# Kernel optimization log

Hardware: AMD Instinct MI355X
Metric: run time of the kernel (lower is better)

The kernel has to match this reference:

```python
import jax, jax.numpy as jnp
import numpy as np

N = 65536      # total nodes (512 graphs x 128 agents)
E = 524288     # total edges (avg degree 8)
NPG = 128      # nodes per graph
OBS = 256      # dim_in_node + dim_in_u
HID = 512      # hidden_dim
MID = 256      # dim_mid
LSTM = 256     # dim_lstm_out
DOUT = 128     # dim_out
DLAST = 128    # dim_last
RFM = 256      # rfm_hidden_dim
LH = 256       # last_hidden
ACT = 8        # act_dims


def setup_inputs() -> dict:
    key = jax.random.key(0)
    ks = jax.random.split(key, 30)

    def rn(k, shape, fan_in):
        return jax.random.normal(k, shape, jnp.float32) * (1.0 / np.sqrt(fan_in))

    src = jax.random.randint(ks[3], (E,), 0, N, jnp.int32)
    # keep edges inside each 128-node graph (batched-graph semantics)
    dst = (src // NPG) * NPG + jax.random.randint(ks[4], (E,), 0, NPG, jnp.int32)

    inp = {
        "obs": jax.random.normal(ks[0], (N, OBS), jnp.float32),
        "h0": jax.random.normal(ks[1], (N, LSTM), jnp.float32) * 0.1,
        "c0": jax.random.normal(ks[2], (N, LSTM), jnp.float32) * 0.1,
        "src": src,
        "dst": dst,
        # mlp1a / mlp1b
        "w1a": rn(ks[5], (HID, OBS), OBS), "b1a": jnp.zeros((HID,), jnp.float32),
        "w1b": rn(ks[6], (MID, HID), HID), "b1b": jnp.zeros((MID,), jnp.float32),
        # lstm1 (gate order i,f,g,o as in torch)
        "w_ih": rn(ks[7], (4 * LSTM, MID), MID), "b_ih": jnp.zeros((4 * LSTM,), jnp.float32),
        "w_hh": rn(ks[8], (4 * LSTM, LSTM), LSTM), "b_hh": jnp.zeros((4 * LSTM,), jnp.float32),
        # mlp1
        "w1": rn(ks[9], (DOUT, LSTM), LSTM), "b1": jnp.zeros((DOUT,), jnp.float32),
        # RFMBlock edge MLP (input = src_nf ++ dst_nf = 2*DOUT; edge_feat/u are 0-dim)
        "we": rn(ks[10], (RFM, 2 * DOUT), 2 * DOUT), "be": jnp.zeros((RFM,), jnp.float32),
        "we2": rn(ks[11], (DLAST, RFM), RFM), "be2": jnp.zeros((DLAST,), jnp.float32),
        # RFMBlock node MLP (input = node_feat ++ h = DOUT + DLAST)
        "wn": rn(ks[12], (RFM, DOUT + DLAST), DOUT + DLAST), "bn": jnp.zeros((RFM,), jnp.float32),
        "wn2": rn(ks[13], (DLAST, RFM), RFM), "bn2": jnp.zeros((DLAST,), jnp.float32),
        # readout
        "wr": rn(ks[14], (LH, DLAST), DLAST), "br": jnp.zeros((LH,), jnp.float32),
        "wr2": rn(ks[15], (ACT, LH), LH), "br2": jnp.zeros((ACT,), jnp.float32),
    }
    return inp


def reference(obs, h0, c0, src, dst,
              w1a, b1a, w1b, b1b, w_ih, b_ih, w_hh, b_hh, w1, b1,
              we, be, we2, be2, wn, bn, wn2, bn2, wr, br, wr2, br2):
    # node encoder: mlp1b(relu(mlp1a(obs)))
    x = jnp.maximum(obs @ w1a.T + b1a, 0.0) @ w1b.T + b1b            # [N, MID]
    # single-step LSTM (batch = N nodes, seq_len = 1)
    gates = x @ w_ih.T + h0 @ w_hh.T + (b_ih + b_hh)                 # [N, 4*LSTM]
    i, f, g, o = jnp.split(gates, 4, axis=-1)
    c1 = jax.nn.sigmoid(f) * c0 + jax.nn.sigmoid(i) * jnp.tanh(g)
    h1 = jax.nn.sigmoid(o) * jnp.tanh(c1)
    nf = jnp.maximum(h1, 0.0) @ w1.T + b1                            # [N, DOUT]

    # RFMBlock edge update: fc_edge2(relu(fc_edge([src_nf, dst_nf])))
    einp = jnp.concatenate([nf[src], nf[dst]], axis=-1)              # [E, 2*DOUT]
    ef = jnp.maximum(einp @ we.T + be, 0.0) @ we2.T + be2            # [E, DLAST]

    # message = edge_feat, reduce = sum over incoming edges (by dst)
    agg = jax.ops.segment_sum(ef, dst, num_segments=N)               # [N, DLAST]

    # RFMBlock node update: fc_node2(relu(fc_node([node_feat, h])))
    ninp = jnp.concatenate([nf, agg], axis=-1)                       # [N, DOUT+DLAST]
    nf2 = jnp.maximum(ninp @ wn.T + bn, 0.0) @ wn2.T + bn2           # [N, DLAST]

    # readout: mlp1_readout2(relu(mlp1_readout(n_out)))
    logits = jnp.maximum(nf2 @ wr.T + br, 0.0) @ wr2.T + br2         # [N, ACT]
    return logits, h1, c1
```

## Files before the change

kernel.cpp:

```cpp
#include <hip/hip_runtime.h>
#include <cstdint>
#include <cstddef>


#define NN 65536
#define NE 524288

typedef __bf16 bf16x8 __attribute__((ext_vector_type(8)));
typedef float  f32x4  __attribute__((ext_vector_type(4)));

typedef __attribute__((address_space(1))) unsigned int glb_uint;
typedef __attribute__((address_space(3))) unsigned int lds_uint;

__device__ __forceinline__ void async16(const void* g, void* l){
  __builtin_amdgcn_global_load_lds((glb_uint*)g, (lds_uint*)l, 16, 0, 0);
}

__device__ __forceinline__ float bf2f(unsigned short u){
  union { unsigned int i; float f; } v; v.i = ((unsigned int)u) << 16; return v.f;
}
__device__ __forceinline__ unsigned short f2b(float f){
  union { float f; unsigned int i; } v; v.f = f;
  unsigned int r = v.i + 0x7FFFu + ((v.i >> 16) & 1u);
  return (unsigned short)(r >> 16);
}
__device__ __forceinline__ float sigm(float x){ return 1.f/(1.f+__expf(-x)); }

struct ConvArgs {
  const float* s[14];
  unsigned short* d[14];
  int n4[14];
  int cnt;
};

__global__ __launch_bounds__(256) void convert_kernel(ConvArgs a){
  int stride = gridDim.x * blockDim.x;
  int gid = blockIdx.x * blockDim.x + threadIdx.x;
  for (int seg = 0; seg < a.cnt; ++seg){
    const float4* s = (const float4*)a.s[seg];
    ushort4* d = (ushort4*)a.d[seg];
    int n4 = a.n4[seg];
    for (int i = gid; i < n4; i += stride){
      float4 v = s[i];
      ushort4 o; o.x=f2b(v.x); o.y=f2b(v.y); o.z=f2b(v.z); o.w=f2b(v.w);
      d[i] = o;
    }
  }
}

template<int ACT, int RSCALE>
__global__ __launch_bounds__(256) void gemm_kernel(
    const unsigned short* __restrict__ A, int lda,
    const unsigned short* __restrict__ B, int ldb, int K,
    const float* __restrict__ bias,
    const int* __restrict__ rs,
    unsigned short* __restrict__ C, int ldc)
{
  __shared__ alignas(16) unsigned short As[2][4096];
  __shared__ alignas(16) unsigned short Bs[2][4096];
  int t = threadIdx.x, wave = t >> 6, lane = t & 63;
  int m0 = blockIdx.x * 128, n0 = blockIdx.y * 128;
  int wr = wave >> 1, wc = wave & 1;

  f32x4 acc[4][4] = {};

  int srow = lane & 15, schunk = lane >> 4;
  const unsigned short* Ap0 = A + (size_t)(m0 + wave * 16 + srow) * lda + schunk * 8;
  const unsigned short* Ap1 = Ap0 + (size_t)64 * lda;
  const unsigned short* Bp0 = B + (size_t)(n0 + wave * 16 + srow) * ldb + schunk * 8;
  const unsigned short* Bp1 = Bp0 + (size_t)64 * ldb;

  auto stage = [&](int b, int kt){
    async16(Ap0 + kt, &As[b][(wave)     << 9]);
    async16(Ap1 + kt, &As[b][(wave + 4) << 9]);
    async16(Bp0 + kt, &Bs[b][(wave)     << 9]);
    async16(Bp1 + kt, &Bs[b][(wave + 4) << 9]);
  };
  int fo = (schunk << 7) + (srow << 3);
  auto compute = [&](int b){
    bf16x8 av[4], bv[4];
#pragma unroll
    for (int m = 0; m < 4; ++m) av[m] = *(const bf16x8*)&As[b][((wr * 4 + m) << 9) + fo];
#pragma unroll
    for (int n = 0; n < 4; ++n) bv[n] = *(const bf16x8*)&Bs[b][((wc * 4 + n) << 9) + fo];
#pragma unroll
    for (int m = 0; m < 4; ++m)
#pragma unroll
      for (int n = 0; n < 4; ++n)
        acc[m][n] = __builtin_amdgcn_mfma_f32_16x16x32_bf16(av[m], bv[n], acc[m][n], 0, 0, 0);
  };

  stage(0, 0);
  asm volatile("s_waitcnt vmcnt(0)" ::: "memory");
  __builtin_amdgcn_s_barrier();
  int cur = 0;
  for (int kt = 32; kt < K; kt += 32){
    stage(cur ^ 1, kt);
    asm volatile("s_waitcnt vmcnt(4)" ::: "memory");
    __builtin_amdgcn_sched_barrier(0);
    __builtin_amdgcn_s_barrier();
    compute(cur);
    asm volatile("s_waitcnt lgkmcnt(0)" ::: "memory");
    __builtin_amdgcn_s_barrier();
    cur ^= 1;
  }
  asm volatile("s_waitcnt vmcnt(0)" ::: "memory");
  __builtin_amdgcn_sched_barrier(0);
  __builtin_amdgcn_s_barrier();
  compute(cur);

  int coll = lane & 15, rq = lane >> 4;
#pragma unroll
  for (int n = 0; n < 4; ++n){
    int col = n0 + wc * 64 + n * 16 + coll;
    float bv = bias[col];
#pragma unroll
    for (int m = 0; m < 4; ++m){
#pragma unroll
      for (int r = 0; r < 4; ++r){
        int rrow = m0 + wr * 64 + m * 16 + rq * 4 + r;
        float scale = RSCALE ? (float)rs[rrow] : 1.0f;
        float v = acc[m][n][r] + bv * scale;
        if (ACT) v = fmaxf(v, 0.f);
        C[(size_t)rrow * ldc + col] = f2b(v);
      }
    }
  }
}

__global__ __launch_bounds__(256) void gates_lstm_kernel(
    const unsigned short* __restrict__ Xb,
    const unsigned short* __restrict__ H0b,
    const unsigned short* __restrict__ Wih,
    const unsigned short* __restrict__ Whh,
    const float* __restrict__ b_ih, const float* __restrict__ b_hh,
    const float* __restrict__ c0,
    float* __restrict__ h1o, float* __restrict__ c1o,
    unsigned short* __restrict__ rb)
{
  __shared__ alignas(16) unsigned short As[2][2048];
  __shared__ alignas(16) unsigned short Bs[2][4][2048];
  int t = threadIdx.x, wave = t >> 6, lane = t & 63;
  int m0 = blockIdx.x * 64, cb = blockIdx.y * 64;
  int srow = lane & 15, schunk = lane >> 4;

  f32x4 acc[4][4] = {};

  auto stage = [&](int b, int kt){
    const unsigned short* Abase = (kt < 256) ? (Xb + kt) : (H0b + (kt - 256));
    const unsigned short* Wbase = (kt < 256) ? (Wih + kt) : (Whh + (kt - 256));
    async16(Abase + (size_t)(m0 + wave * 16 + srow) * 256 + schunk * 8, &As[b][wave << 9]);
#pragma unroll
    for (int g = 0; g < 4; ++g)
      async16(Wbase + (size_t)(g * 256 + cb + wave * 16 + srow) * 256 + schunk * 8,
              &Bs[b][g][wave << 9]);
  };
  int fo = (schunk << 7) + (srow << 3);
  auto compute = [&](int b){
    bf16x8 a = *(const bf16x8*)&As[b][(wave << 9) + fo];
#pragma unroll
    for (int g = 0; g < 4; ++g){
#pragma unroll
      for (int j = 0; j < 4; ++j){
        bf16x8 bb = *(const bf16x8*)&Bs[b][g][(j << 9) + fo];
        acc[g][j] = __builtin_amdgcn_mfma_f32_16x16x32_bf16(a, bb, acc[g][j], 0, 0, 0);
      }
    }
  };

  stage(0, 0);
  asm volatile("s_waitcnt vmcnt(0)" ::: "memory");
  __builtin_amdgcn_s_barrier();
  int cur = 0;
  for (int kt = 32; kt < 512; kt += 32){
    stage(cur ^ 1, kt);
    asm volatile("s_waitcnt vmcnt(5)" ::: "memory");
    __builtin_amdgcn_sched_barrier(0);
    __builtin_amdgcn_s_barrier();
    compute(cur);
    asm volatile("s_waitcnt lgkmcnt(0)" ::: "memory");
    __builtin_amdgcn_s_barrier();
    cur ^= 1;
  }
  asm volatile("s_waitcnt vmcnt(0)" ::: "memory");
  __builtin_amdgcn_sched_barrier(0);
  __builtin_amdgcn_s_barrier();
  compute(cur);

  int coll = lane & 15, rq = lane >> 4;
#pragma unroll
  for (int j = 0; j < 4; ++j){
    int col = cb + j * 16 + coll;
    float bi  = b_ih[col]       + b_hh[col];
    float bff = b_ih[256 + col] + b_hh[256 + col];
    float bg  = b_ih[512 + col] + b_hh[512 + col];
    float bo  = b_ih[768 + col] + b_hh[768 + col];
#pragma unroll
    for (int r = 0; r < 4; ++r){
      int node = m0 + wave * 16 + rq * 4 + r;
      size_t off = (size_t)node * 256 + col;
      float iv = sigm(acc[0][j][r] + bi);
      float fv = sigm(acc[1][j][r] + bff);
      float gv = tanhf(acc[2][j][r] + bg);
      float ov = sigm(acc[3][j][r] + bo);
      float cv = fv * c0[off] + iv * gv;
      float hv = ov * tanhf(cv);
      h1o[off] = hv;
      c1o[off] = cv;
      rb[off] = f2b(fmaxf(hv, 0.f));
    }
  }
}

__global__ __launch_bounds__(256) void hist_kernel(
    const int* __restrict__ dst, int* __restrict__ hist)
{
  int e = blockIdx.x * 256 + threadIdx.x;
  atomicAdd(&hist[dst[e]], 1);
}

__global__ __launch_bounds__(256) void scan1_kernel(
    const int* __restrict__ hist, int* __restrict__ offs, int* __restrict__ bsum)
{
  __shared__ int s[256];
  int b = blockIdx.x, t = threadIdx.x;
  int v = hist[b * 256 + t];
  s[t] = v; __syncthreads();
  for (int d = 1; d < 256; d <<= 1){
    int x = (t >= d) ? s[t - d] : 0;
    __syncthreads();
    s[t] += x;
    __syncthreads();
  }
  offs[b * 256 + t] = s[t] - v;
  if (t == 255) bsum[b] = s[255];
}

__global__ __launch_bounds__(256) void scan2_kernel(int* __restrict__ bsum){
  __shared__ int s[256];
  int t = threadIdx.x;
  int v = bsum[t];
  s[t] = v; __syncthreads();
  for (int d = 1; d < 256; d <<= 1){
    int x = (t >= d) ? s[t - d] : 0;
    __syncthreads();
    s[t] += x;
    __syncthreads();
  }
  bsum[t] = s[t] - v;
}

__global__ __launch_bounds__(256) void scan3_kernel(
    int* __restrict__ offs, const int* __restrict__ bsum, int* __restrict__ cursor)
{
  int i = blockIdx.x * 256 + threadIdx.x;
  int v = offs[i] + bsum[blockIdx.x];
  offs[i] = v;
  cursor[i] = v;
}

__global__ __launch_bounds__(256) void scatter_kernel(
    const int* __restrict__ src, const int* __restrict__ dst,
    int* __restrict__ cursor, int* __restrict__ sorted_src)
{
  int e = blockIdx.x * 256 + threadIdx.x;
  int d = dst[e];
  int pos = atomicAdd(&cursor[d], 1);
  sorted_src[pos] = src[e];
}

__global__ __launch_bounds__(256) void edge_agg_kernel(
    const unsigned short* __restrict__ P,
    const unsigned short* __restrict__ Q,
    const int* __restrict__ sorted_src,
    const int* __restrict__ offs,
    const int* __restrict__ cnt,
    unsigned short* __restrict__ Hsum)
{
  int t = threadIdx.x;
  int n = (blockIdx.x << 2) + (t >> 6);
  int lane = t & 63;
  int d0 = lane * 4;
  int off = offs[n], c = cnt[n];
  ushort4 qv = *(const ushort4*)&Q[(size_t)n * 256 + d0];
  float q0 = bf2f(qv.x), q1 = bf2f(qv.y), q2 = bf2f(qv.z), q3 = bf2f(qv.w);
  float a0 = 0.f, a1 = 0.f, a2 = 0.f, a3 = 0.f;
  for (int i = 0; i < c; ++i){
    int s = sorted_src[off + i];
    ushort4 pv = *(const ushort4*)&P[(size_t)s * 256 + d0];
    a0 += fmaxf(bf2f(pv.x) + q0, 0.f);
    a1 += fmaxf(bf2f(pv.y) + q1, 0.f);
    a2 += fmaxf(bf2f(pv.z) + q2, 0.f);
    a3 += fmaxf(bf2f(pv.w) + q3, 0.f);
  }
  ushort4 o; o.x = f2b(a0); o.y = f2b(a1); o.z = f2b(a2); o.w = f2b(a3);
  *(ushort4*)&Hsum[(size_t)n * 256 + d0] = o;
}

__global__ __launch_bounds__(256) void logits_kernel(
    const unsigned short* __restrict__ rh,
    const unsigned short* __restrict__ wr2b,
    const float* __restrict__ br2,
    float* __restrict__ out)
{
  __shared__ alignas(16) unsigned short W[2048];
  int t = threadIdx.x;
  *(uint4*)&W[t * 8] = *(const uint4*)&wr2b[t * 8];
  __syncthreads();
  int node = blockIdx.x * 32 + (t >> 3);
  int o = t & 7;
  const unsigned short* r = rh + (size_t)node * 256;
  float s = br2[o];
#pragma unroll
  for (int k = 0; k < 256; k += 8){
    uint4 av = *(const uint4*)&r[k];
    const unsigned short* ap = (const unsigned short*)&av;
#pragma unroll
    for (int i = 0; i < 8; ++i) s += bf2f(ap[i]) * bf2f(W[o * 256 + k + i]);
  }
  out[(size_t)node * 8 + o] = s;
}

extern "C" void kernel_launch(void* const* d_in, const int* in_sizes, int n_in,
                              void* d_out, int out_size, void* d_ws, size_t ws_size,
                              hipStream_t stream)
{
  (void)in_sizes; (void)n_in; (void)out_size; (void)ws_size;
  const float* obs = (const float*)d_in[0];
  const float* h0  = (const float*)d_in[1];
  const float* c0  = (const float*)d_in[2];
  const int*   src = (const int*)d_in[3];
  const int*   dst = (const int*)d_in[4];
  const float* w1a = (const float*)d_in[5];
  const float* b1a = (const float*)d_in[6];
  const float* w1b = (const float*)d_in[7];
  const float* b1b = (const float*)d_in[8];
  const float* wih = (const float*)d_in[9];
  const float* bih = (const float*)d_in[10];
  const float* whh = (const float*)d_in[11];
  const float* bhh = (const float*)d_in[12];
  const float* w1  = (const float*)d_in[13];
  const float* b1  = (const float*)d_in[14];
  const float* we  = (const float*)d_in[15];
  const float* be  = (const float*)d_in[16];
  const float* we2 = (const float*)d_in[17];
  const float* be2 = (const float*)d_in[18];
  const float* wn  = (const float*)d_in[19];
  const float* bn  = (const float*)d_in[20];
  const float* wn2 = (const float*)d_in[21];
  const float* bn2 = (const float*)d_in[22];
  const float* wr  = (const float*)d_in[23];
  const float* br  = (const float*)d_in[24];
  const float* wr2 = (const float*)d_in[25];
  const float* br2 = (const float*)d_in[26];

  char* ws = (char*)d_ws;
  typedef unsigned short u16;
  u16* w1a_b = (u16*)(ws + 0);
  u16* w1b_b = (u16*)(ws + 262144);
  u16* wih_b = (u16*)(ws + 524288);
  u16* whh_b = (u16*)(ws + 1048576);
  u16* w1_b  = (u16*)(ws + 1572864);
  u16* we_b  = (u16*)(ws + 1638400);
  u16* we2_b = (u16*)(ws + 1769472);
  u16* wn_b  = (u16*)(ws + 1835008);
  u16* wn2_b = (u16*)(ws + 1966080);
  u16* wr_b  = (u16*)(ws + 2031616);
  u16* wr2_b = (u16*)(ws + 2097152);
  float* zbias = (float*)(ws + 2101248);
  int* hist    = (int*)(ws + 2103296);
  int* offs    = (int*)(ws + 2365440);
  int* cursor  = (int*)(ws + 2627584);
  int* bsum    = (int*)(ws + 2889728);
  int* ssrc    = (int*)(ws + 2890752);

  char* RA = ws + 5242880;
  char* RB = ws + 38797312;
  char* RY = ws + 72351744;

  u16* obs_b = (u16*)RA;
  u16* x_b   = (u16*)RA;
  u16* P     = (u16*)RA;
  u16* nf2   = (u16*)RA;
  u16* h0_b  = (u16*)RB;
  u16* Hsum  = (u16*)RB;
  u16* hidn  = (u16*)RB;
  u16* rh    = (u16*)RB;
  u16* y1    = (u16*)RY;
  u16* rb    = (u16*)RY;
  u16* Q     = (u16*)RY;
  u16* ninp  = (u16*)(RY + 33554432);

  float* logits = (float*)d_out;
  float* h1o = logits + (size_t)NN * 8;
  float* c1o = h1o + (size_t)NN * 256;

  (void)hipMemsetAsync(zbias, 0, 2048, stream);
  (void)hipMemsetAsync(hist, 0, 65536 * 4, stream);

  ConvArgs ca;
  const float* ss[13] = {obs, h0, w1a, w1b, wih, whh, w1, we, we2, wn, wn2, wr, wr2};
  u16* dd[13] = {obs_b, h0_b, w1a_b, w1b_b, wih_b, whh_b, w1_b, we_b, we2_b, wn_b, wn2_b, wr_b, wr2_b};
  int nn[13] = {NN*256, NN*256, 512*256, 256*512, 1024*256, 1024*256, 128*256,
                256*256, 128*256, 256*256, 128*256, 256*128, 8*256};
  for (int i = 0; i < 13; ++i){ ca.s[i]=ss[i]; ca.d[i]=dd[i]; ca.n4[i]=nn[i]/4; }
  ca.cnt = 13;
  convert_kernel<<<2048, 256, 0, stream>>>(ca);

  hist_kernel<<<NE/256, 256, 0, stream>>>(dst, hist);
  scan1_kernel<<<256, 256, 0, stream>>>(hist, offs, bsum);
  scan2_kernel<<<1, 256, 0, stream>>>(bsum);
  scan3_kernel<<<256, 256, 0, stream>>>(offs, bsum, cursor);
  scatter_kernel<<<NE/256, 256, 0, stream>>>(src, dst, cursor, ssrc);

  gemm_kernel<1,0><<<dim3(NN/128, 4), 256, 0, stream>>>(obs_b, 256, w1a_b, 256, 256, b1a, nullptr, y1, 512);
  gemm_kernel<0,0><<<dim3(NN/128, 2), 256, 0, stream>>>(y1, 512, w1b_b, 512, 512, b1b, nullptr, x_b, 256);
  gates_lstm_kernel<<<dim3(NN/64, 4), 256, 0, stream>>>(
      x_b, h0_b, wih_b, whh_b, bih, bhh, c0, h1o, c1o, rb);
  gemm_kernel<0,0><<<dim3(NN/128, 1), 256, 0, stream>>>(rb, 256, w1_b, 256, 256, b1, nullptr, ninp, 256);
  gemm_kernel<0,0><<<dim3(NN/128, 2), 256, 0, stream>>>(ninp, 256, we_b, 256, 128, zbias, nullptr, P, 256);
  gemm_kernel<0,0><<<dim3(NN/128, 2), 256, 0, stream>>>(ninp, 256, we_b + 128, 256, 128, be, nullptr, Q, 256);
  edge_agg_kernel<<<NN/4, 256, 0, stream>>>(P, Q, ssrc, offs, hist, Hsum);
  gemm_kernel<0,1><<<dim3(NN/128, 1), 256, 0, stream>>>(Hsum, 256, we2_b, 256, 256, be2, hist, ninp + 128, 256);
  gemm_kernel<1,0><<<dim3(NN/128, 2), 256, 0, stream>>>(ninp, 256, wn_b, 256, 256, bn, nullptr, hidn, 256);
  gemm_kernel<0,0><<<dim3(NN/128, 1), 256, 0, stream>>>(hidn, 256, wn2_b, 256, 256, bn2, nullptr, nf2, 128);
  gemm_kernel<1,0><<<dim3(NN/128, 2), 256, 0, stream>>>(nf2, 128, wr_b, 128, 128, br, nullptr, rh, 256);
  logits_kernel<<<NN/32, 256, 0, stream>>>(rh, wr2_b, br2, logits);
}
```

Before: 907.4 us.

## Prepack LSTM weights into MFMA fragment layout and drop LDS staging

Adds a pack kernel that converts W_ih and W_hh to bf16 in a layout that matches the per-lane MFMA B-fragment order. The gates/LSTM kernel then loads A and B fragments directly from global memory with contiguous per-wave reads, removing the LDS double buffer, the async copies and the barriers. This trades explicit shared-memory reuse for reliance on L1/L2 caching of the weights, which every block rereads, and adds one small extra launch.

```diff
diff --git a/kernel.cpp b/kernel.cpp
--- a/kernel.cpp
+++ b/kernel.cpp
@@ -44,6 +44,37 @@
       float4 v = s[i];
       ushort4 o; o.x=f2b(v.x); o.y=f2b(v.y); o.z=f2b(v.z); o.w=f2b(v.w);
       d[i] = o;
+    }
+  }
+}
+
+struct PackArgs {
+  const float* s[4];
+  unsigned short* d[4];
+  int n8[4];
+  int ksh[4];
+  int cnt;
+};
+
+__global__ __launch_bounds__(256) void pack_kernel(PackArgs a){
+  int stride = gridDim.x * blockDim.x;
+  int gid0 = blockIdx.x * blockDim.x + threadIdx.x;
+  for (int seg = 0; seg < a.cnt; ++seg){
+    const float* s = a.s[seg];
+    unsigned short* d = a.d[seg];
+    int n8 = a.n8[seg], ksh = a.ksh[seg];
+    int K = 32 << ksh, kmask = (1 << ksh) - 1;
+    for (int gid = gid0; gid < n8; gid += stride){
+      int f = gid >> 6, l = gid & 63;
+      int c16 = f >> ksh, ks = f & kmask;
+      size_t soff = (size_t)((c16 << 4) + (l & 15)) * K + (ks << 5) + ((l >> 4) << 3);
+      float4 v0 = *(const float4*)(s + soff);
+      float4 v1 = *(const float4*)(s + soff + 4);
+      ushort4 o0, o1;
+      o0.x=f2b(v0.x); o0.y=f2b(v0.y); o0.z=f2b(v0.z); o0.w=f2b(v0.w);
+      o1.x=f2b(v1.x); o1.y=f2b(v1.y); o1.z=f2b(v1.z); o1.w=f2b(v1.w);
+      *(ushort4*)(d + (size_t)gid * 8)     = o0;
+      *(ushort4*)(d + (size_t)gid * 8 + 4) = o1;
     }
   }
 }
@@ -131,61 +162,46 @@
 __global__ __launch_bounds__(256) void gates_lstm_kernel(
     const unsigned short* __restrict__ Xb,
     const unsigned short* __restrict__ H0b,
-    const unsigned short* __restrict__ Wih,
-    const unsigned short* __restrict__ Whh,
+    const unsigned short* __restrict__ Wip,
+    const unsigned short* __restrict__ Whp,
     const float* __restrict__ b_ih, const float* __restrict__ b_hh,
     const float* __restrict__ c0,
     float* __restrict__ h1o, float* __restrict__ c1o,
     unsigned short* __restrict__ rb)
 {
-  __shared__ alignas(16) unsigned short As[2][2048];
-  __shared__ alignas(16) unsigned short Bs[2][4][2048];
   int t = threadIdx.x, wave = t >> 6, lane = t & 63;
   int m0 = blockIdx.x * 64, cb = blockIdx.y * 64;
-  int srow = lane & 15, schunk = lane >> 4;
+  int l15 = lane & 15, l4 = lane >> 4;
+  int cb16 = cb >> 4;
+  int lofs = lane << 3;
 
   f32x4 acc[4][4] = {};
 
-  auto stage = [&](int b, int kt){
-    const unsigned short* Abase = (kt < 256) ? (Xb + kt) : (H0b + (kt - 256));
-    const unsigned short* Wbase = (kt < 256) ? (Wih + kt) : (Whh + (kt - 256));
-    async16(Abase + (size_t)(m0 + wave * 16 + srow) * 256 + schunk * 8, &As[b][wave << 9]);
+  const unsigned short* Ax = Xb  + (size_t)(m0 + wave * 16 + l15) * 256 + (l4 << 3);
+  const unsigned short* Ah = H0b + (size_t)(m0 + wave * 16 + l15) * 256 + (l4 << 3);
+
+#pragma unroll
+  for (int ks = 0; ks < 8; ++ks){
+    bf16x8 a = *(const bf16x8*)(Ax + (ks << 5));
 #pragma unroll
     for (int g = 0; g < 4; ++g)
-      async16(Wbase + (size_t)(g * 256 + cb + wave * 16 + srow) * 256 + schunk * 8,
-              &Bs[b][g][wave << 9]);
-  };
-  int fo = (schunk << 7) + (srow << 3);
-  auto compute = [&](int b){
-    bf16x8 a = *(const bf16x8*)&As[b][(wave << 9) + fo];
-#pragma unroll
-    for (int g = 0; g < 4; ++g){
 #pragma unroll
       for (int j = 0; j < 4; ++j){
-        bf16x8 bb = *(const bf16x8*)&Bs[b][g][(j << 9) + fo];
-        acc[g][j] = __builtin_amdgcn_mfma_f32_16x16x32_bf16(a, bb, acc[g][j], 0, 0, 0);
+        bf16x8 b = *(const bf16x8*)(Wip + ((size_t)((g * 16 + cb16 + j) * 8 + ks) << 9) + lofs);
+        acc[g][j] = __builtin_amdgcn_mfma_f32_16x16x32_bf16(a, b, acc[g][j], 0, 0, 0);
       }
-    }
-  };
-
-  stage(0, 0);
-  asm volatile("s_waitcnt vmcnt(0)" ::: "memory");
-  __builtin_amdgcn_s_barrier();
-  int cur = 0;
-  for (int kt = 32; kt < 512; kt += 32){
-    stage(cur ^ 1, kt);
-    asm volatile("s_waitcnt vmcnt(5)" ::: "memory");
-    __builtin_amdgcn_sched_barrier(0);
-    __builtin_amdgcn_s_barrier();
-    compute(cur);
-    asm volatile("s_waitcnt lgkmcnt(0)" ::: "memory");
-    __builtin_amdgcn_s_barrier();
-    cur ^= 1;
-  }
-  asm volatile("s_waitcnt vmcnt(0)" ::: "memory");
-  __builtin_amdgcn_sched_barrier(0);
-  __builtin_amdgcn_s_barrier();
-  compute(cur);
+  }
+#pragma unroll
+  for (int ks = 0; ks < 8; ++ks){
+    bf16x8 a = *(const bf16x8*)(Ah + (ks << 5));
+#pragma unroll
+    for (int g = 0; g < 4; ++g)
+#pragma unroll
+      for (int j = 0; j < 4; ++j){
+        bf16x8 b = *(const bf16x8*)(Whp + ((size_t)((g * 16 + cb16 + j) * 8 + ks) << 9) + lofs);
+        acc[g][j] = __builtin_amdgcn_mfma_f32_16x16x32_bf16(a, b, acc[g][j], 0, 0, 0);
+      }
+  }
 
   int coll = lane & 15, rq = lane >> 4;
 #pragma unroll
@@ -358,8 +374,8 @@
   typedef unsigned short u16;
   u16* w1a_b = (u16*)(ws + 0);
   u16* w1b_b = (u16*)(ws + 262144);
-  u16* wih_b = (u16*)(ws + 524288);
-  u16* whh_b = (u16*)(ws + 1048576);
+  u16* wih_p = (u16*)(ws + 524288);
+  u16* whh_p = (u16*)(ws + 1048576);
   u16* w1_b  = (u16*)(ws + 1572864);
   u16* we_b  = (u16*)(ws + 1638400);
   u16* we2_b = (u16*)(ws + 1769472);
@@ -399,13 +415,19 @@
   (void)hipMemsetAsync(hist, 0, 65536 * 4, stream);
 
   ConvArgs ca;
-  const float* ss[13] = {obs, h0, w1a, w1b, wih, whh, w1, we, we2, wn, wn2, wr, wr2};
-  u16* dd[13] = {obs_b, h0_b, w1a_b, w1b_b, wih_b, whh_b, w1_b, we_b, we2_b, wn_b, wn2_b, wr_b, wr2_b};
-  int nn[13] = {NN*256, NN*256, 512*256, 256*512, 1024*256, 1024*256, 128*256,
+  const float* ss[11] = {obs, h0, w1a, w1b, w1, we, we2, wn, wn2, wr, wr2};
+  u16* dd[11] = {obs_b, h0_b, w1a_b, w1b_b, w1_b, we_b, we2_b, wn_b, wn2_b, wr_b, wr2_b};
+  int nn[11] = {NN*256, NN*256, 512*256, 256*512, 128*256,
                 256*256, 128*256, 256*256, 128*256, 256*128, 8*256};
-  for (int i = 0; i < 13; ++i){ ca.s[i]=ss[i]; ca.d[i]=dd[i]; ca.n4[i]=nn[i]/4; }
-  ca.cnt = 13;
+  for (int i = 0; i < 11; ++i){ ca.s[i]=ss[i]; ca.d[i]=dd[i]; ca.n4[i]=nn[i]/4; }
+  ca.cnt = 11;
   convert_kernel<<<2048, 256, 0, stream>>>(ca);
+
+  PackArgs pa;
+  pa.s[0] = wih; pa.d[0] = wih_p; pa.n8[0] = 1024*256/8; pa.ksh[0] = 3;
+  pa.s[1] = whh; pa.d[1] = whh_p; pa.n8[1] = 1024*256/8; pa.ksh[1] = 3;
+  pa.cnt = 2;
+  pack_kernel<<<512, 256, 0, stream>>>(pa);
 
   hist_kernel<<<NE/256, 256, 0, stream>>>(dst, hist);
   scan1_kernel<<<256, 256, 0, stream>>>(hist, offs, bsum);
@@ -416,7 +438,7 @@
   gemm_kernel<1,0><<<dim3(NN/128, 4), 256, 0, stream>>>(obs_b, 256, w1a_b, 256, 256, b1a, nullptr, y1, 512);
   gemm_kernel<0,0><<<dim3(NN/128, 2), 256, 0, stream>>>(y1, 512, w1b_b, 512, 512, b1b, nullptr, x_b, 256);
   gates_lstm_kernel<<<dim3(NN/64, 4), 256, 0, stream>>>(
-      x_b, h0_b, wih_b, whh_b, bih, bhh, c0, h1o, c1o, rb);
+      x_b, h0_b, wih_p, whh_p, bih, bhh, c0, h1o, c1o, rb);
   gemm_kernel<0,0><<<dim3(NN/128, 1), 256, 0, stream>>>(rb, 256, w1_b, 256, 256, b1, nullptr, ninp, 256);
   gemm_kernel<0,0><<<dim3(NN/128, 2), 256, 0, stream>>>(ninp, 256, we_b, 256, 128, zbias, nullptr, P, 256);
   gemm_kernel<0,0><<<dim3(NN/128, 2), 256, 0, stream>>>(ninp, 256, we_b + 128, 256, 128, be, nullptr, Q, 256);
```

Result: slower. 1.355 ms (+49.3%).
